# Performance work log

Hardware: AMD Instinct MI355X
Metric: run time of the kernel (lower is better)

Reference implementation:

```python
import jax, jax.numpy as jnp
import numpy as np

N = 50000   # nodes
E = 800000  # edges (avg degree 16)
H = 3       # attention heads
D_IN, D_HID, D_OUT = 256, 64, 10


def setup_inputs() -> dict:
    key = jax.random.key(0)
    ks = jax.random.split(key, 8)
    x = jax.random.normal(ks[0], (N, D_IN), dtype=jnp.float32)
    edge_index = jax.random.randint(ks[1], (2, E), 0, N, dtype=jnp.int64)
    W1 = jax.random.normal(ks[2], (H, D_IN, D_HID), dtype=jnp.float32) / np.sqrt(D_IN)
    a_src1 = jax.random.normal(ks[3], (H, D_HID), dtype=jnp.float32) / np.sqrt(D_HID)
    a_dst1 = jax.random.normal(ks[4], (H, D_HID), dtype=jnp.float32) / np.sqrt(D_HID)
    W2 = jax.random.normal(ks[5], (H, D_HID, D_OUT), dtype=jnp.float32) / np.sqrt(D_HID)
    a_src2 = jax.random.normal(ks[6], (H, D_OUT), dtype=jnp.float32) / np.sqrt(D_OUT)
    a_dst2 = jax.random.normal(ks[7], (H, D_OUT), dtype=jnp.float32) / np.sqrt(D_OUT)
    return {"x": x, "edge_index": edge_index, "W1": W1, "a_src1": a_src1,
            "a_dst1": a_dst1, "W2": W2, "a_src2": a_src2, "a_dst2": a_dst2}


def gat_layer(x, src, dst, W, a_s, a_d, n):
    # x: [N, Din]; W: [H, Din, Dout]; returns [N, Dout] (heads averaged)
    z = jnp.einsum('nd,hde->nhe', x, W)                     # [N, H, Dout]
    e_src = jnp.einsum('nhe,he->nh', z, a_s)[src]           # [E, H]
    e_dst = jnp.einsum('nhe,he->nh', z, a_d)[dst]           # [E, H]
    e = jax.nn.leaky_relu(e_src + e_dst, 0.2)               # [E, H]
    # numerically-stable softmax over incoming edges of each dst node
    m = jax.lax.stop_gradient(jax.ops.segment_max(e, dst, num_segments=n))
    ex = jnp.exp(e - m[dst])                                # [E, H]
    denom = jax.ops.segment_sum(ex, dst, num_segments=n)    # [N, H]
    alpha = ex / (denom[dst] + 1e-16)                       # [E, H]
    out = jax.ops.segment_sum(z[src] * alpha[:, :, None], dst, num_segments=n)
    return out.mean(axis=1)                                 # [N, Dout]


def reference(x, edge_index, W1, a_src1, a_dst1, W2, a_src2, a_dst2):
    n = x.shape[0]
    src, dst = edge_index[0], edge_index[1]
    # dropout layers are identity in eval/deterministic mode
    h = gat_layer(x, src, dst, W1, a_src1, a_dst1, n)
    h = jax.nn.elu(h)
    h = gat_layer(h, src, dst, W2, a_src2, a_dst2, n)
    return h, jax.nn.log_softmax(h, axis=1)
```

## Files before the change

kernel.cpp:

```cpp
#include <hip/hip_runtime.h>
#include <math.h>

#define DIN  256
#define DHID 64
#define NH   3
#define DOUT 10
#define CAP  64

typedef __attribute__((ext_vector_type(8))) short bf16x8;
typedef __attribute__((ext_vector_type(4))) float f32x4;

__device__ inline unsigned short f2bf(float f) {
    unsigned u = __builtin_bit_cast(unsigned, f);
    unsigned r = (u + 0x7FFFu + ((u >> 16) & 1u)) >> 16;
    return (unsigned short)r;
}
__device__ inline float bf2f(unsigned short s) {
    unsigned u = ((unsigned)s) << 16;
    return __builtin_bit_cast(float, u);
}
__device__ inline f32x4 cvt4(ushort4 z) {
    f32x4 r;
    r[0] = bf2f(z.x); r[1] = bf2f(z.y); r[2] = bf2f(z.z); r[3] = bf2f(z.w);
    return r;
}


__global__ __launch_bounds__(256) void scatter_repack_kernel(
        const int* __restrict__ src, const int* __restrict__ dst,
        int* __restrict__ cursor, int* __restrict__ esrcp, int E, int scatBlocks,
        const float* __restrict__ W1, unsigned short* __restrict__ W1p) {
    if ((int)blockIdx.x < scatBlocks) {
        int i = (blockIdx.x * 256 + threadIdx.x) * 4;
        if (i + 3 < E) {
            int4 s4 = *(const int4*)(src + i);
            int4 d4 = *(const int4*)(dst + i);
            int p0 = atomicAdd(cursor + d4.x, 1);
            int p1 = atomicAdd(cursor + d4.y, 1);
            int p2 = atomicAdd(cursor + d4.z, 1);
            int p3 = atomicAdd(cursor + d4.w, 1);
            if (p0 < CAP) esrcp[d4.x * CAP + p0] = s4.x;
            if (p1 < CAP) esrcp[d4.y * CAP + p1] = s4.y;
            if (p2 < CAP) esrcp[d4.z * CAP + p2] = s4.z;
            if (p3 < CAP) esrcp[d4.w * CAP + p3] = s4.w;
        } else {
            for (int k = i; k < E; ++k) {
                int d = dst[k];
                int pos = atomicAdd(cursor + d, 1);
                if (pos < CAP) esrcp[d * CAP + pos] = src[k];
            }
        }
    } else {
        int idx = (blockIdx.x - scatBlocks) * 256 + threadIdx.x;
        if (idx < 49152) {
            int j = idx & 7, l = (idx >> 3) & 63, q = (idx >> 9) & 7, t = idx >> 12;
            int c = t * 16 + (l & 15);
            int k = q * 32 + (l >> 4) * 8 + j;
            int h = c >> 6, jj = c & 63;
            W1p[idx] = f2bf(W1[h * 16384 + k * 64 + jj]);
        }
    }
}


__global__ __launch_bounds__(128) void gemm1_mfma_kernel(const float* __restrict__ x,
                                                         const bf16x8* __restrict__ W1p,
                                                         const float* __restrict__ a_s,
                                                         const float* __restrict__ a_d,
                                                         unsigned short* __restrict__ z1bf,
                                                         float* __restrict__ s1,
                                                         float* __restrict__ d1, int n) {
    __shared__ unsigned short Xs[32][272];
    int tid = threadIdx.x;
    int w = tid >> 6, lane = tid & 63;
    int m = lane & 15, quad = lane >> 4;
    int n0 = blockIdx.x * 32;

    for (int i = tid; i < 2048; i += 128) {
        int r = i >> 6, c4 = i & 63;
        int nn = n0 + r;
        float4 a = (nn < n) ? *(const float4*)(x + (size_t)nn * 256 + c4 * 4)
                            : (float4){0.f, 0.f, 0.f, 0.f};
        ushort4 b;
        b.x = f2bf(a.x); b.y = f2bf(a.y); b.z = f2bf(a.z); b.w = f2bf(a.w);
        *(ushort4*)(&Xs[r][c4 * 4]) = b;
    }
    __syncthreads();

    int rloc = w * 16 + m;
    f32x4 acc[12];
    #pragma unroll
    for (int t = 0; t < 12; ++t) acc[t] = (f32x4){0.f, 0.f, 0.f, 0.f};
    #pragma unroll
    for (int q = 0; q < 8; ++q) {
        bf16x8 af = *(const bf16x8*)(&Xs[rloc][q * 32 + quad * 8]);
        #pragma unroll
        for (int t = 0; t < 12; ++t) {
            bf16x8 bfr = W1p[(t * 8 + q) * 64 + lane];
            acc[t] = __builtin_amdgcn_mfma_f32_16x16x32_bf16(af, bfr, acc[t], 0, 0, 0);
        }
    }
    __syncthreads();

    float as_r[12], ad_r[12];
    #pragma unroll
    for (int t = 0; t < 12; ++t) { as_r[t] = a_s[t * 16 + m]; ad_r[t] = a_d[t * 16 + m]; }

    #pragma unroll
    for (int reg = 0; reg < 4; ++reg) {
        int row_loc = w * 16 + quad * 4 + reg;
        int row_out = n0 + row_loc;
        bool ok = row_out < n;
        float ps[3] = {0.f, 0.f, 0.f}, pd[3] = {0.f, 0.f, 0.f};
        #pragma unroll
        for (int t = 0; t < 12; ++t) {
            float v = acc[t][reg];
            Xs[row_loc][t * 16 + m] = f2bf(v);
            ps[t >> 2] += v * as_r[t];
            pd[t >> 2] += v * ad_r[t];
        }
        #pragma unroll
        for (int h = 0; h < 3; ++h) {
            float s = ps[h], d = pd[h];
            #pragma unroll
            for (int msk = 1; msk < 16; msk <<= 1) {
                s += __shfl_xor(s, msk, 16);
                d += __shfl_xor(d, msk, 16);
            }
            if (ok && m == 0) { s1[row_out * 4 + h] = s; d1[row_out * 4 + h] = d; }
        }
    }
    __syncthreads();

    for (int i = tid; i < 1536; i += 128) {
        int r = i / 48, c4 = i % 48;
        int nn = n0 + r;
        if (nn < n)
            *(ushort4*)(z1bf + (size_t)nn * 192 + c4 * 4) = *(const ushort4*)(&Xs[r][c4 * 4]);
    }
}


__global__ __launch_bounds__(256) void agg1_kernel(const int* __restrict__ cnts,
                                                   const int* __restrict__ esrcp,
                                                   const float* __restrict__ s1,
                                                   const float* __restrict__ d1,
                                                   const unsigned short* __restrict__ z1bf,
                                                   float* __restrict__ h1, int n) {
    __shared__ float wlds[4][196];
    int tid = threadIdx.x;
    int lane = tid & 63, wave = tid >> 6;
    int v = blockIdx.x * 4 + wave;
    if (v >= n) return;
    int cnt = cnts[v]; if (cnt > CAP) cnt = CAP;
    int m16 = lane & 15;
    int grp = lane >> 4;
    int head = grp > 2 ? 2 : grp;
    bool rowact = lane < 48;
    float dv0 = d1[v * 4], dv1 = d1[v * 4 + 1], dv2 = d1[v * 4 + 2];
    float* wl = wlds[wave];

    int u_l = 0; float w0 = 0.f, w1 = 0.f, w2 = 0.f;
    if (lane < cnt) {
        u_l = esrcp[v * CAP + lane];
        float4 sv = *(const float4*)(s1 + (size_t)u_l * 4);
        float e0 = sv.x + dv0; e0 = e0 > 0.f ? e0 : 0.2f * e0;
        float e1 = sv.y + dv1; e1 = e1 > 0.f ? e1 : 0.2f * e1;
        float e2 = sv.z + dv2; e2 = e2 > 0.f ? e2 : 0.2f * e2;
        w0 = __expf(e0); w1 = __expf(e1); w2 = __expf(e2);
    }
    wl[lane] = w0; wl[65 + lane] = w1; wl[130 + lane] = w2;
    float4 wv = *(const float4*)(&wl[head * 65 + m16 * 4]);
    float denp = wv.x + wv.y + wv.z + wv.w;
    #pragma unroll
    for (int msk = 1; msk < 16; msk <<= 1) denp += __shfl_xor(denp, msk, 16);

    f32x4 acc = (f32x4){0.f, 0.f, 0.f, 0.f};
    if (rowact) {
        int rnd = (cnt + 3) & ~3;
        const int wb = head * 65;
        for (int j = 0; j < rnd; j += 4) {
            int u0 = __builtin_amdgcn_readlane(u_l, j);
            int u1 = __builtin_amdgcn_readlane(u_l, j + 1);
            int u2 = __builtin_amdgcn_readlane(u_l, j + 2);
            int u3 = __builtin_amdgcn_readlane(u_l, j + 3);
            float wa = wl[wb + j], wb2 = wl[wb + j + 1];
            float wc = wl[wb + j + 2], wd = wl[wb + j + 3];
            ushort4 za = *(const ushort4*)(z1bf + (size_t)u0 * 192 + lane * 4);
            ushort4 zb = *(const ushort4*)(z1bf + (size_t)u1 * 192 + lane * 4);
            ushort4 zc = *(const ushort4*)(z1bf + (size_t)u2 * 192 + lane * 4);
            ushort4 zd = *(const ushort4*)(z1bf + (size_t)u3 * 192 + lane * 4);
            acc += cvt4(za) * wa;
            acc += cvt4(zb) * wb2;
            acc += cvt4(zc) * wc;
            acc += cvt4(zd) * wd;
        }
    }
    float invd = (1.f / 3.f) / (denp + 1e-16f);
    float acc0 = rowact ? acc[0] * invd : 0.f;
    float acc1 = rowact ? acc[1] * invd : 0.f;
    float acc2 = rowact ? acc[2] * invd : 0.f;
    float acc3 = rowact ? acc[3] * invd : 0.f;
    acc0 += __shfl_down(acc0, 32, 64); acc0 += __shfl_down(acc0, 16, 64);
    acc1 += __shfl_down(acc1, 32, 64); acc1 += __shfl_down(acc1, 16, 64);
    acc2 += __shfl_down(acc2, 32, 64); acc2 += __shfl_down(acc2, 16, 64);
    acc3 += __shfl_down(acc3, 32, 64); acc3 += __shfl_down(acc3, 16, 64);
    if (lane < 16) {
        float4 o;
        o.x = acc0 > 0.f ? acc0 : __expf(acc0) - 1.f;
        o.y = acc1 > 0.f ? acc1 : __expf(acc1) - 1.f;
        o.z = acc2 > 0.f ? acc2 : __expf(acc2) - 1.f;
        o.w = acc3 > 0.f ? acc3 : __expf(acc3) - 1.f;
        *(float4*)(h1 + (size_t)v * 64 + lane * 4) = o;
    }
}


__global__ __launch_bounds__(256) void gemm2_kernel(const float* __restrict__ h1,
                                                    const float* __restrict__ W2,
                                                    const float* __restrict__ as2,
                                                    const float* __restrict__ ad2,
                                                    unsigned short* __restrict__ z2bf,
                                                    float* __restrict__ s2,
                                                    float* __restrict__ d2, int n) {
    __shared__ float Xs[32][65];
    __shared__ float Ws[64][32];
    __shared__ float Zs[32][33];
    int tid = threadIdx.x;
    int tx = tid % 32, ty = tid / 32;
    int n0 = blockIdx.x * 32;
    for (int idx = tid; idx < 64 * 32; idx += 256) {
        int kk = idx >> 5, c = idx & 31;
        float wv = 0.f;
        if (c < 30) {
            int h = c / 10, j = c % 10;
            wv = W2[(h * 64 + kk) * 10 + j];
        }
        Ws[kk][c] = wv;
    }
    for (int idx = tid; idx < 32 * 64; idx += 256) {
        int r = idx >> 6, kk = idx & 63;
        int nn = n0 + r;
        Xs[r][kk] = (nn < n) ? h1[(size_t)nn * 64 + kk] : 0.f;
    }
    __syncthreads();
    float acc[4] = {0.f, 0.f, 0.f, 0.f};
    #pragma unroll 8
    for (int kk = 0; kk < 64; ++kk) {
        float w = Ws[kk][tx];
        #pragma unroll
        for (int p = 0; p < 4; ++p) acc[p] += Xs[ty + 8 * p][kk] * w;
    }
    #pragma unroll
    for (int p = 0; p < 4; ++p) {
        int rloc = ty + 8 * p;
        int nn = n0 + rloc;
        float val = tx < 30 ? acc[p] : 0.f;
        Zs[rloc][tx] = val;
        if (nn < n) z2bf[(size_t)nn * 32 + tx] = f2bf(val);
    }
    __syncthreads();
    if (tid < 96) {
        int rloc = tid / 3, h = tid % 3;
        int nn = n0 + rloc;
        if (nn < n) {
            float ss = 0.f, dd = 0.f;
            #pragma unroll
            for (int j = 0; j < 10; ++j) {
                float z = Zs[rloc][h * 10 + j];
                ss += z * as2[h * 10 + j];
                dd += z * ad2[h * 10 + j];
            }
            s2[nn * 4 + h] = ss;
            d2[nn * 4 + h] = dd;
        }
    }
}


__global__ __launch_bounds__(256) void agg2_kernel(const int* __restrict__ cnts,
                                                   const int* __restrict__ esrcp,
                                                   const float* __restrict__ s2,
                                                   const float* __restrict__ d2,
                                                   const unsigned short* __restrict__ z2bf,
                                                   float* __restrict__ out, int n) {
    __shared__ float wlds[4][196];
    __shared__ float dlds[4][4];
    int tid = threadIdx.x;
    int lane = tid & 63, wave = tid >> 6;
    int v = blockIdx.x * 4 + wave;
    if (v >= n) return;
    int cnt = cnts[v]; if (cnt > CAP) cnt = CAP;
    int c2 = lane & 15;
    int quad = lane >> 4;
    int headc = c2 < 5 ? 0 : (c2 < 10 ? 1 : 2);
    int headg = quad > 2 ? 2 : quad;
    float dv0 = d2[v * 4], dv1 = d2[v * 4 + 1], dv2 = d2[v * 4 + 2];
    float* wl = wlds[wave];

    int u_l = 0; float w0 = 0.f, w1 = 0.f, w2 = 0.f;
    if (lane < cnt) {
        u_l = esrcp[v * CAP + lane];
        float4 sv = *(const float4*)(s2 + (size_t)u_l * 4);
        float e0 = sv.x + dv0; e0 = e0 > 0.f ? e0 : 0.2f * e0;
        float e1 = sv.y + dv1; e1 = e1 > 0.f ? e1 : 0.2f * e1;
        float e2 = sv.z + dv2; e2 = e2 > 0.f ? e2 : 0.2f * e2;
        w0 = __expf(e0); w1 = __expf(e1); w2 = __expf(e2);
    }
    wl[lane] = w0; wl[65 + lane] = w1; wl[130 + lane] = w2;
    float4 wv = *(const float4*)(&wl[headg * 65 + c2 * 4]);
    float denp = wv.x + wv.y + wv.z + wv.w;
    #pragma unroll
    for (int msk = 1; msk < 16; msk <<= 1) denp += __shfl_xor(denp, msk, 16);
    if (c2 == 0 && quad < 3) dlds[wave][quad] = denp;

    float ax = 0.f, ay = 0.f;
    int rnd = (cnt + 3) & ~3;
    const int wb = headc * 65;
    for (int j = 0; j < rnd; j += 4) {
        int u = __shfl(u_l, j + quad, 64);
        float w = wl[wb + j + quad];
        ushort2 z = *(const ushort2*)(z2bf + (size_t)u * 32 + c2 * 2);
        ax += w * bf2f(z.x);
        ay += w * bf2f(z.y);
    }
    float den = dlds[wave][headc];
    ax += __shfl_down(ax, 32, 64); ax += __shfl_down(ax, 16, 64);
    ay += __shfl_down(ay, 32, 64); ay += __shfl_down(ay, 16, 64);
    float inv = 1.f / (den + 1e-16f);
    float rx = ax * inv, ry = ay * inv;
    float rx5  = __shfl(rx, lane + 5, 64);
    float rx10 = __shfl(rx, lane + 10, 64);
    float ry5  = __shfl(ry, lane + 5, 64);
    float ry10 = __shfl(ry, lane + 10, 64);
    float rrx = (rx + rx5 + rx10) * (1.f / 3.f);
    float rry = (ry + ry5 + ry10) * (1.f / 3.f);
    bool act = lane < 5;
    float mx = act ? fmaxf(rrx, rry) : -1e30f;
    #pragma unroll
    for (int msk = 1; msk < 8; msk <<= 1) mx = fmaxf(mx, __shfl_xor(mx, msk, 8));
    float e = act ? (__expf(rrx - mx) + __expf(rry - mx)) : 0.f;
    #pragma unroll
    for (int msk = 1; msk < 8; msk <<= 1) e += __shfl_xor(e, msk, 8);
    float lg = __logf(e);
    if (act) {
        float2 o1; o1.x = rrx; o1.y = rry;
        float2 o2; o2.x = rrx - mx - lg; o2.y = rry - mx - lg;
        *(float2*)(out + (size_t)v * DOUT + c2 * 2) = o1;
        *(float2*)(out + (size_t)n * DOUT + (size_t)v * DOUT + c2 * 2) = o2;
    }
}


extern "C" void kernel_launch(void* const* d_in, const int* in_sizes, int n_in,
                              void* d_out, int out_size, void* d_ws, size_t ws_size,
                              hipStream_t stream) {
    const float* x   = (const float*)d_in[0];
    const int*   ei  = (const int*)d_in[1];
    const float* W1  = (const float*)d_in[2];
    const float* as1 = (const float*)d_in[3];
    const float* ad1 = (const float*)d_in[4];
    const float* W2  = (const float*)d_in[5];
    const float* as2 = (const float*)d_in[6];
    const float* ad2 = (const float*)d_in[7];
    float* out = (float*)d_out;

    const int N = in_sizes[0] / DIN;
    const int E = in_sizes[1] / 2;
    const int* src = ei;
    const int* dst = ei + E;

    char* p = (char*)d_ws;
    auto alloc = [&](size_t bytes) -> void* {
        void* r = (void*)p;
        p += (bytes + 255) & ~(size_t)255;
        return r;
    };
    int* cursor  = (int*)alloc((size_t)N * 4);
    int* esrcp   = (int*)alloc((size_t)N * CAP * 4);
    unsigned short* W1p  = (unsigned short*)alloc((size_t)49152 * 2);
    unsigned short* z1bf = (unsigned short*)alloc((size_t)N * 192 * 2);
    float* s1    = (float*)alloc((size_t)N * 4 * 4);
    float* d1    = (float*)alloc((size_t)N * 4 * 4);
    float* h1    = (float*)alloc((size_t)N * 64 * 4);
    unsigned short* z2bf = (unsigned short*)alloc((size_t)N * 32 * 2);
    float* s2    = (float*)alloc((size_t)N * 4 * 4);
    float* d2    = (float*)alloc((size_t)N * 4 * 4);
    (void)alloc(512);

    hipMemsetAsync(cursor, 0, (size_t)N * 4, stream);

    int scatBlocks = (E + 1023) / 1024;
    int repackBlocks = (49152 + 255) / 256;
    scatter_repack_kernel<<<scatBlocks + repackBlocks, 256, 0, stream>>>(
        src, dst, cursor, esrcp, E, scatBlocks, W1, W1p);

    gemm1_mfma_kernel<<<(N + 31) / 32, 128, 0, stream>>>(x, (const bf16x8*)W1p, as1, ad1,
                                                         z1bf, s1, d1, N);
    agg1_kernel<<<(N + 3) / 4, 256, 0, stream>>>(cursor, esrcp, s1, d1, z1bf, h1, N);
    gemm2_kernel<<<(N + 31) / 32, 256, 0, stream>>>(h1, W2, as2, ad2, z2bf, s2, d2, N);
    agg2_kernel<<<(N + 3) / 4, 256, 0, stream>>>(cursor, esrcp, s2, d2, z2bf, out, N);
}
```

Baseline: 261.1 us.

## Fuse edge scatter into GEMM1 launch and zero cursor inside repack kernel

```diff
diff --git a/kernel.cpp b/kernel.cpp
--- a/kernel.cpp
+++ b/kernel.cpp
@@ -26,57 +26,50 @@
 }
 
 
-__global__ __launch_bounds__(256) void scatter_repack_kernel(
+__global__ __launch_bounds__(256) void repack_zero_kernel(const float* __restrict__ W1,
+                                                          unsigned short* __restrict__ W1p,
+                                                          int* __restrict__ cursor, int N) {
+    int bid = blockIdx.x;
+    int tid = threadIdx.x;
+    if (bid < 192) {
+        int idx = bid * 256 + tid;
+        int j = idx & 7, l = (idx >> 3) & 63, q = (idx >> 9) & 7, t = idx >> 12;
+        int c = t * 16 + (l & 15);
+        int k = q * 32 + (l >> 4) * 8 + j;
+        int h = c >> 6, jj = c & 63;
+        W1p[idx] = f2bf(W1[h * 16384 + k * 64 + jj]);
+    } else {
+        int i = (bid - 192) * 256 + tid;
+        if (i < N) cursor[i] = 0;
+    }
+}
+
+
+__global__ __launch_bounds__(256) void gemm1_scatter_kernel(
+        const float* __restrict__ x, const bf16x8* __restrict__ W1p,
+        const float* __restrict__ a_s, const float* __restrict__ a_d,
+        unsigned short* __restrict__ z1bf,
+        float* __restrict__ s1, float* __restrict__ d1, int n, int G,
         const int* __restrict__ src, const int* __restrict__ dst,
-        int* __restrict__ cursor, int* __restrict__ esrcp, int E, int scatBlocks,
-        const float* __restrict__ W1, unsigned short* __restrict__ W1p) {
-    if ((int)blockIdx.x < scatBlocks) {
-        int i = (blockIdx.x * 256 + threadIdx.x) * 4;
-        if (i + 3 < E) {
-            int4 s4 = *(const int4*)(src + i);
-            int4 d4 = *(const int4*)(dst + i);
-            int p0 = atomicAdd(cursor + d4.x, 1);
-            int p1 = atomicAdd(cursor + d4.y, 1);
-            int p2 = atomicAdd(cursor + d4.z, 1);
-            int p3 = atomicAdd(cursor + d4.w, 1);
-            if (p0 < CAP) esrcp[d4.x * CAP + p0] = s4.x;
-            if (p1 < CAP) esrcp[d4.y * CAP + p1] = s4.y;
-            if (p2 < CAP) esrcp[d4.z * CAP + p2] = s4.z;
-            if (p3 < CAP) esrcp[d4.w * CAP + p3] = s4.w;
-        } else {
-            for (int k = i; k < E; ++k) {
-                int d = dst[k];
-                int pos = atomicAdd(cursor + d, 1);
-                if (pos < CAP) esrcp[d * CAP + pos] = src[k];
-            }
-        }
-    } else {
-        int idx = (blockIdx.x - scatBlocks) * 256 + threadIdx.x;
-        if (idx < 49152) {
-            int j = idx & 7, l = (idx >> 3) & 63, q = (idx >> 9) & 7, t = idx >> 12;
-            int c = t * 16 + (l & 15);
-            int k = q * 32 + (l >> 4) * 8 + j;
-            int h = c >> 6, jj = c & 63;
-            W1p[idx] = f2bf(W1[h * 16384 + k * 64 + jj]);
-        }
-    }
-}
-
-
-__global__ __launch_bounds__(128) void gemm1_mfma_kernel(const float* __restrict__ x,
-                                                         const bf16x8* __restrict__ W1p,
-                                                         const float* __restrict__ a_s,
-                                                         const float* __restrict__ a_d,
-                                                         unsigned short* __restrict__ z1bf,
-                                                         float* __restrict__ s1,
-                                                         float* __restrict__ d1, int n) {
-    __shared__ unsigned short Xs[32][272];
-    int tid = threadIdx.x;
+        int* __restrict__ cursor, int* __restrict__ esrcp, int E) {
+    __shared__ unsigned short Xs[64][272];
+    int bid = blockIdx.x;
+    int tid = threadIdx.x;
+    if (bid >= G) {
+        int i = (bid - G) * 256 + tid;
+        if (i < E) {
+            int d = dst[i];
+            int s = src[i];
+            int pos = atomicAdd(cursor + d, 1);
+            if (pos < CAP) esrcp[d * CAP + pos] = s;
+        }
+        return;
+    }
     int w = tid >> 6, lane = tid & 63;
     int m = lane & 15, quad = lane >> 4;
-    int n0 = blockIdx.x * 32;
-
-    for (int i = tid; i < 2048; i += 128) {
+    int n0 = bid * 64;
+
+    for (int i = tid; i < 4096; i += 256) {
         int r = i >> 6, c4 = i & 63;
         int nn = n0 + r;
         float4 a = (nn < n) ? *(const float4*)(x + (size_t)nn * 256 + c4 * 4)
@@ -132,7 +125,7 @@
     }
     __syncthreads();
 
-    for (int i = tid; i < 1536; i += 128) {
+    for (int i = tid; i < 3072; i += 256) {
         int r = i / 48, c4 = i % 48;
         int nn = n0 + r;
         if (nn < n)
@@ -388,15 +381,14 @@
     float* d2    = (float*)alloc((size_t)N * 4 * 4);
     (void)alloc(512);
 
-    hipMemsetAsync(cursor, 0, (size_t)N * 4, stream);
-
-    int scatBlocks = (E + 1023) / 1024;
-    int repackBlocks = (49152 + 255) / 256;
-    scatter_repack_kernel<<<scatBlocks + repackBlocks, 256, 0, stream>>>(
-        src, dst, cursor, esrcp, E, scatBlocks, W1, W1p);
-
-    gemm1_mfma_kernel<<<(N + 31) / 32, 128, 0, stream>>>(x, (const bf16x8*)W1p, as1, ad1,
-                                                         z1bf, s1, d1, N);
+    repack_zero_kernel<<<192 + (N + 255) / 256, 256, 0, stream>>>(W1, W1p, cursor, N);
+
+    int G = (N + 63) / 64;
+    int S = (E + 255) / 256;
+    gemm1_scatter_kernel<<<G + S, 256, 0, stream>>>(
+        x, (const bf16x8*)W1p, as1, ad1, z1bf, s1, d1, N, G,
+        src, dst, cursor, esrcp, E);
+
     agg1_kernel<<<(N + 3) / 4, 256, 0, stream>>>(cursor, esrcp, s1, d1, z1bf, h1, N);
     gemm2_kernel<<<(N + 31) / 32, 256, 0, stream>>>(h1, W2, as2, ad2, z2bf, s2, d2, N);
     agg2_kernel<<<(N + 3) / 4, 256, 0, stream>>>(cursor, esrcp, s2, d2, z2bf, out, N);
```

New measurement: 275.5 us. +5.5%, slower.
